# Kernel tuning notes

Hardware: AMD Instinct MI355X
Metric: run time of the kernel (lower is better)

The kernel has to match this reference:

```python
import jax, jax.numpy as jnp
import numpy as np

B, C, T, H, W = 2, 256, 16, 64, 64
CK = C // 8  # query/key channels = 32


def setup_inputs() -> dict:
    key = jax.random.key(0)
    ks = jax.random.split(key, 4)
    s = 1.0 / np.sqrt(C)
    return {
        "x": jax.random.normal(ks[0], (B, C, T, H, W), dtype=jnp.float32),
        "Wq": jax.random.normal(ks[1], (CK, C), dtype=jnp.float32) * s,
        "bq": jnp.zeros((CK,), dtype=jnp.float32),
        "Wk": jax.random.normal(ks[2], (CK, C), dtype=jnp.float32) * s,
        "bk": jnp.zeros((CK,), dtype=jnp.float32),
        "Wv": jax.random.normal(ks[3], (C, C), dtype=jnp.float32) * s,
        "bv": jnp.zeros((C,), dtype=jnp.float32),
        "gamma": jnp.zeros((1,), dtype=jnp.float32),
    }


def reference(x, Wq, bq, Wk, bk, Wv, bv, gamma):
    b, c, t, h, w = x.shape
    n = t * h * w
    xf = x.reshape(b, c, n)  # [b, C, N]; 1x1 Conv3d == channel matmul
    key = jnp.einsum('dc,bcn->bdn', Wk, xf) + bk[None, :, None]   # [b, CK, N]
    key = jax.nn.softmax(key, axis=2)                              # softmax over spatial
    value = jnp.einsum('ec,bcn->ben', Wv, xf) + bv[None, :, None]  # [b, C, N]
    context = jnp.einsum('bdn,ben->bde', key, value)               # [b, CK, C]
    query = jnp.einsum('dc,bcn->bdn', Wq, xf) + bq[None, :, None]  # [b, CK, N]
    query = jax.nn.softmax(query, axis=1)                          # softmax over channels
    attention = jnp.einsum('bde,bdn->ben', context, query)         # [b, C, N]
    out = gamma[0] * attention.reshape(b, c, t, h, w) + x
    return out
```

## Files before the change

kernel.cpp:

```cpp
#include <hip/hip_runtime.h>
#include <hip/hip_bf16.h>
#include <cstdint>
#include <cstddef>


constexpr int kB  = 2;
constexpr int kC  = 256;
constexpr int kCK = 32;
constexpr int kN  = 65536;
constexpr int kNCol = kB * kN;

typedef __attribute__((ext_vector_type(8))) short bf8;
typedef __attribute__((ext_vector_type(4))) float f4;

constexpr size_t OFF_KLOG  = 0;
constexpr size_t OFF_QS    = OFF_KLOG  + 4194304;
constexpr size_t OFF_WPACK = OFF_QS    + 4194304;
constexpr size_t OFF_BIAS  = OFF_WPACK + 8192;
constexpr size_t OFF_WVT   = OFF_BIAS  + 64;
constexpr size_t OFF_PMAX  = OFF_WVT   + 65536;
constexpr size_t OFF_PSUM  = OFF_PMAX  + 32768;
constexpr size_t OFF_ROWM  = OFF_PSUM  + 32768;
constexpr size_t OFF_RINV  = OFF_ROWM  + 64;
constexpr size_t OFF_MG    = OFF_RINV  + 64;
constexpr size_t OFF_CTXT  = OFF_MG    + 16384;
constexpr size_t OFF_MPART = OFF_CTXT  + 16384;

static __device__ inline short f2bf(float a) {
    union { __hip_bfloat16 h; short s; } u; u.h = __float2bfloat16(a); return u.s;
}
static __device__ inline unsigned int pack2(float a, float b) {
    union { __hip_bfloat162 h2; unsigned int u; } u;
    u.h2 = __float22bfloat162_rn(float2{a, b});
    return u.u;
}
static __device__ inline bf8 mk_pk(f4 u, f4 v, float rm) {
    bf8 r;
    r[0] = f2bf(__expf(u[0] - rm)); r[1] = f2bf(__expf(u[1] - rm));
    r[2] = f2bf(__expf(u[2] - rm)); r[3] = f2bf(__expf(u[3] - rm));
    r[4] = f2bf(__expf(v[0] - rm)); r[5] = f2bf(__expf(v[1] - rm));
    r[6] = f2bf(__expf(v[2] - rm)); r[7] = f2bf(__expf(v[3] - rm));
    return r;
}

__global__ __launch_bounds__(256) void k0_prep(
    const float* __restrict__ Wq, const float* __restrict__ Wk,
    const float* __restrict__ Wv, const float* __restrict__ bq,
    const float* __restrict__ bk, short* __restrict__ wpack,
    float* __restrict__ biasp, float* __restrict__ WvT) {
    int id = blockIdx.x * 256 + threadIdx.x;
    {
        int d = id >> 8, c = id & 255;
        float v = (d < 32) ? Wk[d * kC + c] : Wq[(d - 32) * kC + c];
        wpack[d * kC + c] = f2bf(v);
    }
#pragma unroll
    for (int j = 0; j < 4; ++j) {
        int k = id * 4 + j;
        int c = k >> 8, e = k & 255;
        WvT[(size_t)c * kC + e] = Wv[(size_t)e * kC + c];
    }
    if (id < 64) biasp[id] = (id < 32) ? bk[id] : bq[id - 32];
}

__global__ __launch_bounds__(256, 4) void pa_proj(
    const float* __restrict__ x, const float* __restrict__ wpack_f,
    const float* __restrict__ biasp,
    float* __restrict__ klog, float* __restrict__ qs,
    float* __restrict__ pmax, float* __restrict__ psum) {
    __shared__ __align__(16) unsigned int lds[128 * 20];
    __shared__ float qex[2][8][16];

    const int t = threadIdx.x;
    const int bid = blockIdx.x;
    const int b = bid >> 9;
    const int n0 = (bid & 511) * 128;
    const int w = t >> 6, l = t & 63;
    const int l15 = l & 15, q = l >> 4;

    const short* wp = (const short*)wpack_f;
    bf8 afrag[8];
#pragma unroll
    for (int ck = 0; ck < 8; ++ck)
        afrag[ck] = *reinterpret_cast<const bf8*>(
            wp + (w * 16 + l15) * 256 + ck * 32 + q * 8);

    f4 acc[8];
#pragma unroll
    for (int nt = 0; nt < 8; ++nt) acc[nt] = (f4)0.f;

    const int nl = t & 127;
    const int chh = (t >> 7) * 16;
    const float* xb = x + (size_t)b * kC * kN + n0 + nl;

    float pre[16];
#pragma unroll
    for (int j = 0; j < 8; ++j) {
        pre[2 * j]     = xb[(size_t)(chh + 2 * j) * kN];
        pre[2 * j + 1] = xb[(size_t)(chh + 2 * j + 1) * kN];
    }
#pragma unroll
    for (int j = 0; j < 8; ++j)
        lds[nl * 20 + ((chh >> 1) + j)] = pack2(pre[2 * j], pre[2 * j + 1]);
    __syncthreads();

    for (int ck = 0; ck < 8; ++ck) {
        if (ck < 7) {
            const float* xc = xb + (size_t)(ck + 1) * 32 * kN;
#pragma unroll
            for (int j = 0; j < 8; ++j) {
                pre[2 * j]     = xc[(size_t)(chh + 2 * j) * kN];
                pre[2 * j + 1] = xc[(size_t)(chh + 2 * j + 1) * kN];
            }
        }
#pragma unroll
        for (int nt = 0; nt < 8; ++nt) {
            bf8 bfrag = *reinterpret_cast<const bf8*>(
                (const short*)lds + (nt * 16 + l15) * 40 + q * 8);
            acc[nt] = __builtin_amdgcn_mfma_f32_16x16x32_bf16(
                afrag[ck], bfrag, acc[nt], 0, 0, 0);
        }
        __syncthreads();
        if (ck < 7) {
#pragma unroll
            for (int j = 0; j < 8; ++j)
                lds[nl * 20 + ((chh >> 1) + j)] =
                    pack2(pre[2 * j], pre[2 * j + 1]);
            __syncthreads();
        }
    }

    const f4 bias = *reinterpret_cast<const f4*>(biasp + w * 16 + q * 4);
    float v[8][4];
#pragma unroll
    for (int nt = 0; nt < 8; ++nt)
#pragma unroll
        for (int r = 0; r < 4; ++r) v[nt][r] = acc[nt][r] + bias[r];

    if (w < 2) {
        float* kp = klog + (size_t)b * kCK * kN + n0 + l15;
#pragma unroll
        for (int nt = 0; nt < 8; ++nt)
#pragma unroll
            for (int r = 0; r < 4; ++r) {
                int d = w * 16 + q * 4 + r;
                kp[(size_t)d * kN + nt * 16] = v[nt][r];
            }
#pragma unroll
        for (int r = 0; r < 4; ++r) {
            float m = v[0][r];
#pragma unroll
            for (int nt = 1; nt < 8; ++nt) m = fmaxf(m, v[nt][r]);
            m = fmaxf(m, __shfl_xor(m, 1)); m = fmaxf(m, __shfl_xor(m, 2));
            m = fmaxf(m, __shfl_xor(m, 4)); m = fmaxf(m, __shfl_xor(m, 8));
            float s = 0.f;
#pragma unroll
            for (int nt = 0; nt < 8; ++nt) s += __expf(v[nt][r] - m);
            s += __shfl_xor(s, 1); s += __shfl_xor(s, 2);
            s += __shfl_xor(s, 4); s += __shfl_xor(s, 8);
            if (l15 == 0) {
                int d = w * 16 + q * 4 + r;
                pmax[(size_t)bid * 32 + d] = m;
                psum[(size_t)bid * 32 + d] = s;
            }
        }
    }

    float mw[8], e[8][4], sw[8];
    if (w >= 2) {
#pragma unroll
        for (int nt = 0; nt < 8; ++nt) {
            float m = fmaxf(fmaxf(v[nt][0], v[nt][1]), fmaxf(v[nt][2], v[nt][3]));
            m = fmaxf(m, __shfl_xor(m, 16));
            m = fmaxf(m, __shfl_xor(m, 32));
            mw[nt] = m;
            if (q == 0) qex[w - 2][nt][l15] = m;
        }
    }
    __syncthreads();
    if (w >= 2) {
#pragma unroll
        for (int nt = 0; nt < 8; ++nt) {
            float m = fmaxf(mw[nt], qex[3 - w][nt][l15]);
            mw[nt] = m;
            float s = 0.f;
#pragma unroll
            for (int r = 0; r < 4; ++r) { e[nt][r] = __expf(v[nt][r] - m); s += e[nt][r]; }
            s += __shfl_xor(s, 16);
            s += __shfl_xor(s, 32);
            sw[nt] = s;
        }
    }
    __syncthreads();
    if (w >= 2 && q == 0) {
#pragma unroll
        for (int nt = 0; nt < 8; ++nt) qex[w - 2][nt][l15] = sw[nt];
    }
    __syncthreads();
    if (w >= 2) {
        float* qp = qs + (size_t)b * kCK * kN + n0 + l15;
#pragma unroll
        for (int nt = 0; nt < 8; ++nt) {
            float inv = 1.0f / (sw[nt] + qex[3 - w][nt][l15]);
#pragma unroll
            for (int r = 0; r < 4; ++r) {
                int dq = (w - 2) * 16 + q * 4 + r;
                qp[(size_t)dq * kN + nt * 16] = e[nt][r] * inv;
            }
        }
    }
}

__global__ __launch_bounds__(1024) void k2_stats(
    const float* __restrict__ pmax, const float* __restrict__ psum,
    float* __restrict__ rowm, float* __restrict__ rowinv) {
    __shared__ float sm[16][64];
    __shared__ float ss[16][64];
    int t = threadIdx.x;
    int bd = t & 63, seg = t >> 6;
    int b = bd >> 5, d = bd & 31;
    int j0 = b * 512 + seg * 32;

    float m = -1e30f;
    for (int j = 0; j < 32; ++j) m = fmaxf(m, pmax[(size_t)(j0 + j) * 32 + d]);
    sm[seg][bd] = m;
    __syncthreads();
    if (t < 64) {
        float mm = -1e30f;
        for (int s = 0; s < 16; ++s) mm = fmaxf(mm, sm[s][t]);
        sm[0][t] = mm;
    }
    __syncthreads();
    float M = sm[0][bd];
    float s0 = 0.f, s1 = 0.f;
    for (int j = 0; j < 32; j += 2) {
        size_t i0 = (size_t)(j0 + j) * 32 + d;
        size_t i1 = i0 + 32;
        s0 += psum[i0] * __expf(pmax[i0] - M);
        s1 += psum[i1] * __expf(pmax[i1] - M);
    }
    ss[seg][bd] = s0 + s1;
    __syncthreads();
    if (t < 64) {
        float S = 0.f;
        for (int s = 0; s < 16; ++s) S += ss[s][t];
        rowm[t] = sm[0][t];
        rowinv[t] = 1.0f / S;
    }
}

__global__ __launch_bounds__(256, 2) void pc_M(
    const float* __restrict__ x, const float* __restrict__ klog,
    const float* __restrict__ rowm, float* __restrict__ Mpart) {
    __shared__ __align__(16) unsigned int lds[256 * 36];

    const int t = threadIdx.x;
    const int bid = blockIdx.x;
    const int b = bid >> 8;
    const int n0 = (bid & 255) * 256;
    const int w = t >> 6, l = t & 63;
    const int l15 = l & 15, q = l >> 4;

    const float rm0 = rowm[b * 32 + l15];
    const float rm1 = rowm[b * 32 + 16 + l15];

    f4 acc[4][2];
#pragma unroll
    for (int i = 0; i < 4; ++i) { acc[i][0] = (f4)0.f; acc[i][1] = (f4)0.f; }

    const int np = t & 31;
    const int cs = t >> 5;
    const float* xb = x + (size_t)b * kC * kN + n0;
    const float* kb = klog + (size_t)b * kCK * kN;

    float2 pre[32];
#pragma unroll
    for (int j = 0; j < 32; ++j)
        pre[j] = *reinterpret_cast<const float2*>(
            xb + (size_t)(cs + 8 * j) * kN + 2 * np);
#pragma unroll
    for (int j = 0; j < 32; ++j)
        lds[(cs + 8 * j) * 36 + np] = pack2(pre[j].x, pre[j].y);
    __syncthreads();

    for (int ch = 0; ch < 4; ++ch) {
        if (ch < 3) {
            const float* xc = xb + (ch + 1) * 64;
#pragma unroll
            for (int j = 0; j < 32; ++j)
                pre[j] = *reinterpret_cast<const float2*>(
                    xc + (size_t)(cs + 8 * j) * kN + 2 * np);
        }
#pragma unroll
        for (int i = 0; i < 2; ++i) {
            const int nwin = n0 + ch * 64 + i * 32;
            const float* kr0 = kb + (size_t)l15 * kN + nwin + q * 8;
            const float* kr1 = kr0 + (size_t)16 * kN;
            f4 u0 = *(const f4*)kr0, u1 = *(const f4*)(kr0 + 4);
            f4 w0 = *(const f4*)kr1, w1 = *(const f4*)(kr1 + 4);
            bf8 a0 = mk_pk(u0, u1, rm0);
            bf8 a1 = mk_pk(w0, w1, rm1);
#pragma unroll
            for (int c4 = 0; c4 < 4; ++c4) {
                int ct = w * 4 + c4;
                bf8 bfr = *reinterpret_cast<const bf8*>(
                    (const short*)lds + (ct * 16 + l15) * 72 + i * 32 + q * 8);
                acc[c4][0] = __builtin_amdgcn_mfma_f32_16x16x32_bf16(
                    a0, bfr, acc[c4][0], 0, 0, 0);
                acc[c4][1] = __builtin_amdgcn_mfma_f32_16x16x32_bf16(
                    a1, bfr, acc[c4][1], 0, 0, 0);
            }
        }
        __syncthreads();
        if (ch < 3) {
#pragma unroll
            for (int j = 0; j < 32; ++j)
                lds[(cs + 8 * j) * 36 + np] = pack2(pre[j].x, pre[j].y);
            __syncthreads();
        }
    }

    float* mp = Mpart + (size_t)bid * (32 * 256);
#pragma unroll
    for (int c4 = 0; c4 < 4; ++c4)
#pragma unroll
        for (int dt = 0; dt < 2; ++dt)
#pragma unroll
            for (int r = 0; r < 4; ++r)
                mp[(dt * 16 + q * 4 + r) * 256 + (w * 4 + c4) * 16 + l15] =
                    acc[c4][dt][r];
}

__global__ __launch_bounds__(256) void k4a_reduce(
    const float* __restrict__ Mpart, float* __restrict__ Mg) {
    int bid = blockIdx.x;
    int b = bid >> 5, seg = bid & 31;
    int idx = seg * 256 + threadIdx.x;
    const float* p = Mpart + (size_t)b * 256 * 8192 + idx;
    float s0 = 0.f, s1 = 0.f, s2 = 0.f, s3 = 0.f;
    for (int j = 0; j < 256; j += 4) {
        s0 += p[(size_t)(j + 0) * 8192];
        s1 += p[(size_t)(j + 1) * 8192];
        s2 += p[(size_t)(j + 2) * 8192];
        s3 += p[(size_t)(j + 3) * 8192];
    }
    Mg[(size_t)b * 8192 + idx] = (s0 + s1) + (s2 + s3);
}

__global__ __launch_bounds__(256) void k4b_ctx(
    const float* __restrict__ Mg, const float* __restrict__ WvT,
    const float* __restrict__ bv, const float* __restrict__ rinv,
    float* __restrict__ ctxT) {
    int bid = blockIdx.x;
    int b = bid >> 5, d = bid & 31;
    int e = threadIdx.x;
    const float* mp = Mg + (size_t)b * 8192 + d * 256;
    float ri = rinv[b * 32 + d];
    float a0 = 0.f, a1 = 0.f, a2 = 0.f, a3 = 0.f;
    for (int c = 0; c < 256; c += 4) {
        a0 = fmaf(mp[c + 0], WvT[(size_t)(c + 0) * kC + e], a0);
        a1 = fmaf(mp[c + 1], WvT[(size_t)(c + 1) * kC + e], a1);
        a2 = fmaf(mp[c + 2], WvT[(size_t)(c + 2) * kC + e], a2);
        a3 = fmaf(mp[c + 3], WvT[(size_t)(c + 3) * kC + e], a3);
    }
    ctxT[((size_t)b * kC + e) * kCK + d] = fmaf(ri, (a0 + a1) + (a2 + a3), bv[e]);
}

__global__ __launch_bounds__(256) void k5_out(
    const float* __restrict__ x, const float* __restrict__ qs,
    const float* __restrict__ ctxT, const float* __restrict__ gamma,
    float* __restrict__ out) {
    int col = blockIdx.x * 256 + threadIdx.x;
    int b = col >> 16;
    int n = col & (kN - 1);
    int bu = __builtin_amdgcn_readfirstlane(b);

    const float* qp = qs + (size_t)bu * kCK * kN + n;
    float qv[kCK];
#pragma unroll
    for (int d = 0; d < kCK; ++d) qv[d] = qp[(size_t)d * kN];

    const float* cp = ctxT + (size_t)bu * kC * kCK;
    const float* xp = x + (size_t)bu * kC * kN + n;
    float* op = out + (size_t)bu * kC * kN + n;
    float g = gamma[0];

    for (int e0 = 0; e0 < kC; e0 += 8) {
        float xv[8];
#pragma unroll
        for (int ee = 0; ee < 8; ++ee) xv[ee] = xp[(size_t)(e0 + ee) * kN];
#pragma unroll
        for (int ee = 0; ee < 8; ++ee) {
            const float* ce = cp + (e0 + ee) * kCK;
            float a0 = 0.f, a1 = 0.f, a2 = 0.f, a3 = 0.f;
#pragma unroll
            for (int d = 0; d < kCK; d += 4) {
                a0 = fmaf(ce[d + 0], qv[d + 0], a0);
                a1 = fmaf(ce[d + 1], qv[d + 1], a1);
                a2 = fmaf(ce[d + 2], qv[d + 2], a2);
                a3 = fmaf(ce[d + 3], qv[d + 3], a3);
            }
            float att = (a0 + a1) + (a2 + a3);
            op[(size_t)(e0 + ee) * kN] = fmaf(g, att, xv[ee]);
        }
    }
}

extern "C" void kernel_launch(void* const* d_in, const int* in_sizes, int n_in,
                              void* d_out, int out_size, void* d_ws, size_t ws_size,
                              hipStream_t stream) {
    const float* x     = (const float*)d_in[0];
    const float* Wq    = (const float*)d_in[1];
    const float* bq    = (const float*)d_in[2];
    const float* Wk    = (const float*)d_in[3];
    const float* bk    = (const float*)d_in[4];
    const float* Wv    = (const float*)d_in[5];
    const float* bv    = (const float*)d_in[6];
    const float* gamma = (const float*)d_in[7];
    float* out = (float*)d_out;
    float* ws  = (float*)d_ws;

    float* klog  = ws + OFF_KLOG;
    float* qsbuf = ws + OFF_QS;
    float* wpack = ws + OFF_WPACK;
    float* biasp = ws + OFF_BIAS;
    float* WvT   = ws + OFF_WVT;
    float* pmax  = ws + OFF_PMAX;
    float* psum  = ws + OFF_PSUM;
    float* rowm  = ws + OFF_ROWM;
    float* rinv  = ws + OFF_RINV;
    float* Mg    = ws + OFF_MG;
    float* ctxT  = ws + OFF_CTXT;
    float* Mpart = ws + OFF_MPART;

    k0_prep<<<64, 256, 0, stream>>>(Wq, Wk, Wv, bq, bk,
                                    (short*)wpack, biasp, WvT);
    pa_proj<<<1024, 256, 0, stream>>>(x, wpack, biasp, klog, qsbuf, pmax, psum);
    k2_stats<<<1, 1024, 0, stream>>>(pmax, psum, rowm, rinv);
    pc_M<<<512, 256, 0, stream>>>(x, klog, rowm, Mpart);
    k4a_reduce<<<64, 256, 0, stream>>>(Mpart, Mg);
    k4b_ctx<<<64, 256, 0, stream>>>(Mg, WvT, bv, rinv, ctxT);
    k5_out<<<512, 256, 0, stream>>>(x, qsbuf, ctxT, gamma, out);
}
```

Before: 371.1 us.

## Store query softmax and key exponentials as bf16, split output kernel by channel groups

Query softmax results are written as bf16 instead of fp32, halving that intermediate buffer's traffic. A new kernel precomputes exp(key - rowmax) as packed bf16 once, so pc_M loads ready MFMA operands instead of recomputing exponentials from fp32 logits. The output kernel is split across four channel groups to launch more blocks, at the cost of re-reading the query vector per group. This adds an extra launch and pass over klog, and lowers query precision.

```diff
diff --git a/kernel.cpp b/kernel.cpp
--- a/kernel.cpp
+++ b/kernel.cpp
@@ -8,14 +8,15 @@
 constexpr int kC  = 256;
 constexpr int kCK = 32;
 constexpr int kN  = 65536;
-constexpr int kNCol = kB * kN;
 
 typedef __attribute__((ext_vector_type(8))) short bf8;
 typedef __attribute__((ext_vector_type(4))) float f4;
+typedef __attribute__((ext_vector_type(4))) unsigned int u4;
 
 constexpr size_t OFF_KLOG  = 0;
 constexpr size_t OFF_QS    = OFF_KLOG  + 4194304;
-constexpr size_t OFF_WPACK = OFF_QS    + 4194304;
+constexpr size_t OFF_PK    = OFF_QS    + 2097152;
+constexpr size_t OFF_WPACK = OFF_PK    + 2097152;
 constexpr size_t OFF_BIAS  = OFF_WPACK + 8192;
 constexpr size_t OFF_WVT   = OFF_BIAS  + 64;
 constexpr size_t OFF_PMAX  = OFF_WVT   + 65536;
@@ -29,18 +30,15 @@
 static __device__ inline short f2bf(float a) {
     union { __hip_bfloat16 h; short s; } u; u.h = __float2bfloat16(a); return u.s;
 }
+static __device__ inline float bf2f(short s) {
+    union { float f; unsigned int u; } z;
+    z.u = ((unsigned int)(unsigned short)s) << 16;
+    return z.f;
+}
 static __device__ inline unsigned int pack2(float a, float b) {
     union { __hip_bfloat162 h2; unsigned int u; } u;
     u.h2 = __float22bfloat162_rn(float2{a, b});
     return u.u;
-}
-static __device__ inline bf8 mk_pk(f4 u, f4 v, float rm) {
-    bf8 r;
-    r[0] = f2bf(__expf(u[0] - rm)); r[1] = f2bf(__expf(u[1] - rm));
-    r[2] = f2bf(__expf(u[2] - rm)); r[3] = f2bf(__expf(u[3] - rm));
-    r[4] = f2bf(__expf(v[0] - rm)); r[5] = f2bf(__expf(v[1] - rm));
-    r[6] = f2bf(__expf(v[2] - rm)); r[7] = f2bf(__expf(v[3] - rm));
-    return r;
 }
 
 __global__ __launch_bounds__(256) void k0_prep(
@@ -66,7 +64,7 @@
 __global__ __launch_bounds__(256, 4) void pa_proj(
     const float* __restrict__ x, const float* __restrict__ wpack_f,
     const float* __restrict__ biasp,
-    float* __restrict__ klog, float* __restrict__ qs,
+    float* __restrict__ klog, short* __restrict__ qs,
     float* __restrict__ pmax, float* __restrict__ psum) {
     __shared__ __align__(16) unsigned int lds[128 * 20];
     __shared__ float qex[2][8][16];
@@ -182,7 +180,6 @@
 #pragma unroll
         for (int nt = 0; nt < 8; ++nt) {
             float m = fmaxf(mw[nt], qex[3 - w][nt][l15]);
-            mw[nt] = m;
             float s = 0.f;
 #pragma unroll
             for (int r = 0; r < 4; ++r) { e[nt][r] = __expf(v[nt][r] - m); s += e[nt][r]; }
@@ -198,14 +195,14 @@
     }
     __syncthreads();
     if (w >= 2) {
-        float* qp = qs + (size_t)b * kCK * kN + n0 + l15;
+        short* qp = qs + (size_t)b * kCK * kN + n0 + l15;
 #pragma unroll
         for (int nt = 0; nt < 8; ++nt) {
             float inv = 1.0f / (sw[nt] + qex[3 - w][nt][l15]);
 #pragma unroll
             for (int r = 0; r < 4; ++r) {
                 int dq = (w - 2) * 16 + q * 4 + r;
-                qp[(size_t)dq * kN + nt * 16] = e[nt][r] * inv;
+                qp[(size_t)dq * kN + nt * 16] = f2bf(e[nt][r] * inv);
             }
         }
     }
@@ -249,9 +246,25 @@
     }
 }
 
+__global__ __launch_bounds__(256) void k3_pk(
+    const float* __restrict__ klog, const float* __restrict__ rowm,
+    short* __restrict__ pk) {
+    size_t base = ((size_t)blockIdx.x * 256 + threadIdx.x) * 8;
+    int row = (int)(base >> 16);
+    float rm = rowm[row];
+    f4 u = *reinterpret_cast<const f4*>(klog + base);
+    f4 v = *reinterpret_cast<const f4*>(klog + base + 4);
+    u4 o;
+    o.x = pack2(__expf(u[0] - rm), __expf(u[1] - rm));
+    o.y = pack2(__expf(u[2] - rm), __expf(u[3] - rm));
+    o.z = pack2(__expf(v[0] - rm), __expf(v[1] - rm));
+    o.w = pack2(__expf(v[2] - rm), __expf(v[3] - rm));
+    *reinterpret_cast<u4*>(pk + base) = o;
+}
+
 __global__ __launch_bounds__(256, 2) void pc_M(
-    const float* __restrict__ x, const float* __restrict__ klog,
-    const float* __restrict__ rowm, float* __restrict__ Mpart) {
+    const float* __restrict__ x, const short* __restrict__ pk,
+    float* __restrict__ Mpart) {
     __shared__ __align__(16) unsigned int lds[256 * 36];
 
     const int t = threadIdx.x;
@@ -261,9 +274,6 @@
     const int w = t >> 6, l = t & 63;
     const int l15 = l & 15, q = l >> 4;
 
-    const float rm0 = rowm[b * 32 + l15];
-    const float rm1 = rowm[b * 32 + 16 + l15];
-
     f4 acc[4][2];
 #pragma unroll
     for (int i = 0; i < 4; ++i) { acc[i][0] = (f4)0.f; acc[i][1] = (f4)0.f; }
@@ -271,7 +281,7 @@
     const int np = t & 31;
     const int cs = t >> 5;
     const float* xb = x + (size_t)b * kC * kN + n0;
-    const float* kb = klog + (size_t)b * kCK * kN;
+    const short* kb = pk + (size_t)b * kCK * kN;
 
     float2 pre[32];
 #pragma unroll
@@ -294,12 +304,9 @@
 #pragma unroll
         for (int i = 0; i < 2; ++i) {
             const int nwin = n0 + ch * 64 + i * 32;
-            const float* kr0 = kb + (size_t)l15 * kN + nwin + q * 8;
-            const float* kr1 = kr0 + (size_t)16 * kN;
-            f4 u0 = *(const f4*)kr0, u1 = *(const f4*)(kr0 + 4);
-            f4 w0 = *(const f4*)kr1, w1 = *(const f4*)(kr1 + 4);
-            bf8 a0 = mk_pk(u0, u1, rm0);
-            bf8 a1 = mk_pk(w0, w1, rm1);
+            const short* kr0 = kb + (size_t)l15 * kN + nwin + q * 8;
+            bf8 a0 = *reinterpret_cast<const bf8*>(kr0);
+            bf8 a1 = *reinterpret_cast<const bf8*>(kr0 + (size_t)16 * kN);
 #pragma unroll
             for (int c4 = 0; c4 < 4; ++c4) {
                 int ct = w * 4 + c4;
@@ -367,31 +374,34 @@
 }
 
 __global__ __launch_bounds__(256) void k5_out(
-    const float* __restrict__ x, const float* __restrict__ qs,
+    const float* __restrict__ x, const short* __restrict__ qs,
     const float* __restrict__ ctxT, const float* __restrict__ gamma,
     float* __restrict__ out) {
-    int col = blockIdx.x * 256 + threadIdx.x;
+    int cg = blockIdx.x >> 2;
+    int ec = blockIdx.x & 3;
+    int col = cg * 256 + threadIdx.x;
     int b = col >> 16;
     int n = col & (kN - 1);
     int bu = __builtin_amdgcn_readfirstlane(b);
 
-    const float* qp = qs + (size_t)bu * kCK * kN + n;
+    const short* qp = qs + (size_t)bu * kCK * kN + n;
     float qv[kCK];
 #pragma unroll
-    for (int d = 0; d < kCK; ++d) qv[d] = qp[(size_t)d * kN];
-
+    for (int d = 0; d < kCK; ++d) qv[d] = bf2f(qp[(size_t)d * kN]);
+
+    const int e0b = ec * 64;
     const float* cp = ctxT + (size_t)bu * kC * kCK;
-    const float* xp = x + (size_t)bu * kC * kN + n;
-    float* op = out + (size_t)bu * kC * kN + n;
+    const float* xp = x + (size_t)bu * kC * kN + (size_t)e0b * kN + n;
+    float* op = out + (size_t)bu * kC * kN + (size_t)e0b * kN + n;
     float g = gamma[0];
 
-    for (int e0 = 0; e0 < kC; e0 += 8) {
+    for (int e0 = 0; e0 < 64; e0 += 8) {
         float xv[8];
 #pragma unroll
         for (int ee = 0; ee < 8; ++ee) xv[ee] = xp[(size_t)(e0 + ee) * kN];
 #pragma unroll
         for (int ee = 0; ee < 8; ++ee) {
-            const float* ce = cp + (e0 + ee) * kCK;
+            const float* ce = cp + (e0b + e0 + ee) * kCK;
             float a0 = 0.f, a1 = 0.f, a2 = 0.f, a3 = 0.f;
 #pragma unroll
             for (int d = 0; d < kCK; d += 4) {
@@ -421,7 +431,8 @@
     float* ws  = (float*)d_ws;
 
     float* klog  = ws + OFF_KLOG;
-    float* qsbuf = ws + OFF_QS;
+    short* qsbuf = (short*)(ws + OFF_QS);
+    short* pk    = (short*)(ws + OFF_PK);
     float* wpack = ws + OFF_WPACK;
     float* biasp = ws + OFF_BIAS;
     float* WvT   = ws + OFF_WVT;
@@ -437,8 +448,9 @@
                                     (short*)wpack, biasp, WvT);
     pa_proj<<<1024, 256, 0, stream>>>(x, wpack, biasp, klog, qsbuf, pmax, psum);
     k2_stats<<<1, 1024, 0, stream>>>(pmax, psum, rowm, rinv);
-    pc_M<<<512, 256, 0, stream>>>(x, klog, rowm, Mpart);
+    k3_pk<<<2048, 256, 0, stream>>>(klog, rowm, pk);
+    pc_M<<<512, 256, 0, stream>>>(x, pk, Mpart);
     k4a_reduce<<<64, 256, 0, stream>>>(Mpart, Mg);
     k4b_ctx<<<64, 256, 0, stream>>>(Mg, WvT, bv, rinv, ctxT);
-    k5_out<<<512, 256, 0, stream>>>(x, qsbuf, ctxT, gamma, out);
-}
+    k5_out<<<2048, 256, 0, stream>>>(x, qsbuf, ctxT, gamma, out);
+}
```

Result: faster. 345.2 us (-7.0%).
